# Optimization experiments

Hardware: AMD Instinct MI355X
Metric: run time of the kernel (lower is better)

Reference implementation:

```python
import jax, jax.numpy as jnp
import numpy as np

B, N, M, D, H = 2, 2048, 2048, 1024, 16
HD = D // H          # head_dim = 64
F = int(D * 4.0)     # mlp hidden = 4096
EPS = 1e-5


def layernorm(x, w, b):
    mu = jnp.mean(x, axis=-1, keepdims=True)
    var = jnp.mean(jnp.square(x - mu), axis=-1, keepdims=True)
    return (x - mu) * jax.lax.rsqrt(var + EPS) * w + b


def setup_inputs() -> dict:
    key = jax.random.key(0)
    ks = jax.random.split(key, 8)
    w = lambda k, shape: jax.random.normal(k, shape, dtype=jnp.float32) * 0.02
    return {
        "query": jax.random.normal(ks[0], (B, N, D), dtype=jnp.float32),
        "context": jax.random.normal(ks[1], (B, M, D), dtype=jnp.float32),
        "qpos": jax.random.randint(ks[2], (B, N), 0, N, dtype=jnp.int32),
        "cpos": jax.random.randint(ks[3], (B, M), 0, M, dtype=jnp.int32),
        "Wq_w": w(ks[4], (D, D)), "Wq_b": jnp.zeros((D,), jnp.float32),
        "Wk_w": w(ks[5], (D, D)), "Wk_b": jnp.zeros((D,), jnp.float32),
        "Wv_w": w(ks[6], (D, D)), "Wv_b": jnp.zeros((D,), jnp.float32),
        "qn_w": jnp.ones((HD,), jnp.float32), "qn_b": jnp.zeros((HD,), jnp.float32),
        "kn_w": jnp.ones((HD,), jnp.float32), "kn_b": jnp.zeros((HD,), jnp.float32),
        "ffn_w": jnp.ones((D,), jnp.float32), "ffn_b": jnp.zeros((D,), jnp.float32),
        "fc1_w": w(ks[7], (D, F)), "fc1_b": jnp.zeros((F,), jnp.float32),
        "fc2_w": w(jax.random.fold_in(key, 99), (F, D)), "fc2_b": jnp.zeros((D,), jnp.float32),
    }


def reference(query, context, qpos, cpos,
              Wq_w, Wq_b, Wk_w, Wk_b, Wv_w, Wv_b,
              qn_w, qn_b, kn_w, kn_b,
              ffn_w, ffn_b, fc1_w, fc1_b, fc2_w, fc2_b):
    # rope=None -> qpos/cpos unused (kept for signature fidelity)
    res = query
    # QKV projections, split heads -> (B,H,T,HD)
    Q = (query @ Wq_w + Wq_b).reshape(B, N, H, HD).transpose(0, 2, 1, 3)
    K = (context @ Wk_w + Wk_b).reshape(B, M, H, HD).transpose(0, 2, 1, 3)
    V = (context @ Wv_w + Wv_b).reshape(B, M, H, HD).transpose(0, 2, 1, 3)
    # per-head LayerNorm on q and k
    Q = layernorm(Q, qn_w, qn_b)
    K = layernorm(K, kn_w, kn_b)
    # attention
    scores = jnp.einsum('bhnd,bhmd->bhnm', Q, K) / jnp.sqrt(jnp.float32(HD))
    attn = jax.nn.softmax(scores, axis=-1)
    out = jnp.einsum('bhnm,bhmd->bhnd', attn, V)
    out = out.transpose(0, 2, 1, 3).reshape(B, N, D)
    out = res + out
    # MLP block with pre-norm
    res2 = out
    h = layernorm(out, ffn_w, ffn_b)
    h = jax.nn.gelu(h @ fc1_w + fc1_b, approximate=False)
    h = h @ fc2_w + fc2_b
    return res2 + h
```

## Files before the change

### kernel.cpp

```cpp
#include <hip/hip_runtime.h>
#include <hip/hip_bf16.h>
#include <math.h>

constexpr int Bb  = 2;
constexpr int Nn  = 2048;
constexpr int Mm  = 2048;
constexpr int Dd  = 1024;
constexpr int Hh  = 16;
constexpr int HD  = 64;
constexpr int Ff  = 4096;
constexpr float EPS = 1e-5f;
constexpr float QSCALE = 0.125f * 1.4426950408889634f;
constexpr float SMAX = 12.0f;

typedef __attribute__((ext_vector_type(8))) short bf16x8;
typedef __attribute__((ext_vector_type(4))) short bf16x4;
typedef __attribute__((ext_vector_type(4))) float f32x4;

__device__ inline unsigned short f2bf(float f) {
    __hip_bfloat16 h = __float2bfloat16(f);
    return *reinterpret_cast<unsigned short*>(&h);
}
__device__ inline unsigned short f2bf_rh(float f) {
    union { float f; unsigned u; } c{f};
    return (unsigned short)((c.u + 0x8000u) >> 16);
}
__device__ inline float bf2f(unsigned short u) {
    union { unsigned u; float f; } c{(unsigned)u << 16};
    return c.f;
}

__device__ inline float gelu_fast(float x) {
    float t = x * x;
    float f = fmaf(-0.10295004f, t, -2.30211782f);
    float e = __builtin_amdgcn_exp2f(x * f);
    return x * __builtin_amdgcn_rcpf(1.0f + e);
}

__device__ inline void async_load16(const void* g, void* l) {
    __builtin_amdgcn_global_load_lds(
        (const __attribute__((address_space(1))) void*)g,
        (__attribute__((address_space(3))) void*)l, 16, 0, 0);
}

__device__ inline bf16x8 ld_b64x2(const unsigned short* p) {
    bf16x4 lo = *(const bf16x4*)p;
    bf16x4 hi = *(const bf16x4*)(p + 4);
    bf16x8 r;
#pragma unroll
    for (int i = 0; i < 4; i++) { r[i] = lo[i]; r[i + 4] = hi[i]; }
    return r;
}

__global__ __launch_bounds__(256) void prep_kernel(
    const float* __restrict__ query, const float* __restrict__ context,
    unsigned short* __restrict__ qa, unsigned short* __restrict__ ca,
    const float* __restrict__ W0, const float* __restrict__ W1,
    const float* __restrict__ W2, const float* __restrict__ W3,
    const float* __restrict__ W4,
    unsigned short* __restrict__ T0, unsigned short* __restrict__ T1,
    unsigned short* __restrict__ T2, unsigned short* __restrict__ T3,
    unsigned short* __restrict__ T4)
{
    __shared__ float tile[32][33];
    int bid = blockIdx.x;
    if (bid < 8192) {
        int i = bid * 256 + threadIdx.x;
        const float* x; unsigned short* y; int k;
        if (i < 1048576) { x = query; y = qa; k = i; }
        else { x = context; y = ca; k = i - 1048576; }
        float4 v = reinterpret_cast<const float4*>(x)[k];
        ushort4 o;
        o.x = f2bf(v.x); o.y = f2bf(v.y); o.z = f2bf(v.z); o.w = f2bf(v.w);
        reinterpret_cast<ushort4*>(y)[k] = o;
        return;
    }
    bid -= 8192;
    const float* W; unsigned short* T; int K, Cn, tid;
    if (bid < 3072) {
        int j = bid >> 10; tid = bid & 1023;
        W = (j == 0) ? W0 : (j == 1) ? W1 : W2;
        T = (j == 0) ? T0 : (j == 1) ? T1 : T2;
        K = Dd; Cn = Dd;
    } else if (bid < 7168) {
        tid = bid - 3072; W = W3; T = T3; K = Dd; Cn = Ff;
    } else {
        tid = bid - 7168; W = W4; T = T4; K = Ff; Cn = Dd;
    }
    int xt = Cn >> 5;
    int bx = tid % xt, by = tid / xt;
    int tx = threadIdx.x & 31, ty = threadIdx.x >> 5;
    int c = bx * 32 + tx;
    int kbase = by * 32;
#pragma unroll
    for (int i = ty; i < 32; i += 8)
        tile[i][tx] = W[(size_t)(kbase + i) * Cn + c];
    __syncthreads();
    int k = kbase + tx;
#pragma unroll
    for (int i = ty; i < 32; i += 8)
        T[(size_t)(bx * 32 + i) * K + k] = f2bf(tile[tx][i]);
}

__global__ __launch_bounds__(256) void qkv_fused_kernel(
    const unsigned short* __restrict__ qa, const unsigned short* __restrict__ ca,
    const unsigned short* __restrict__ Wqt, const unsigned short* __restrict__ Wkt,
    const unsigned short* __restrict__ Wvt,
    const float* __restrict__ bq, const float* __restrict__ bk,
    const float* __restrict__ bv,
    const float* __restrict__ qn_w, const float* __restrict__ qn_b,
    const float* __restrict__ kn_w, const float* __restrict__ kn_b,
    unsigned short* __restrict__ Qbh, unsigned short* __restrict__ Kbh,
    unsigned short* __restrict__ Vt_g)
{
    __shared__ __align__(16) unsigned short As[2][128 * 32];
    __shared__ __align__(16) unsigned short Bs[2][128 * 32];

    const int bz = blockIdx.z;
    const unsigned short* A  = (bz == 0) ? qa : ca;
    const unsigned short* Bt = (bz == 0) ? Wqt : (bz == 1) ? Wkt : Wvt;
    const float* bias        = (bz == 0) ? bq  : (bz == 1) ? bk  : bv;
    const int K = Dd;

    const int t    = threadIdx.x;
    const int wave = t >> 6;
    const int lane = t & 63;
    const int r0 = blockIdx.y * 128;
    const int c0 = blockIdx.x * 128;
    const int wm = (wave >> 1) * 64;
    const int wn = (wave & 1) * 64;

    f32x4 acc[4][4];
#pragma unroll
    for (int i = 0; i < 4; i++)
#pragma unroll
        for (int j = 0; j < 4; j++) acc[i][j] = (f32x4)0.0f;

    const int row1 = t >> 2;
    const int kcs  = ((t & 3) ^ ((t >> 3) & 3)) * 8;
    const size_t arow1 = (size_t)(r0 + row1) * K + kcs;
    const size_t arow2 = (size_t)(r0 + row1 + 64) * K + kcs;
    const size_t brow1 = (size_t)(c0 + row1) * K + kcs;
    const size_t brow2 = (size_t)(c0 + row1 + 64) * K + kcs;
    char* A1_0 = (char*)&As[0][0] + wave * 1024;
    char* A2_0 = (char*)&As[0][0] + 4096 + wave * 1024;
    char* B1_0 = (char*)&Bs[0][0] + wave * 1024;
    char* B2_0 = (char*)&Bs[0][0] + 4096 + wave * 1024;
    char* A1_1 = (char*)&As[1][0] + wave * 1024;
    char* A2_1 = (char*)&As[1][0] + 4096 + wave * 1024;
    char* B1_1 = (char*)&Bs[1][0] + wave * 1024;
    char* B2_1 = (char*)&Bs[1][0] + 4096 + wave * 1024;

    const int m   = lane & 15;
    const int swc = ((lane >> 4) ^ ((m >> 1) & 3)) << 3;

    async_load16(A + arow1, A1_0);
    async_load16(A + arow2, A2_0);
    async_load16(Bt + brow1, B1_0);
    async_load16(Bt + brow2, B2_0);

    for (int k0 = 0; k0 < K; k0 += 32) {
        __syncthreads();
        const int cur = (k0 >> 5) & 1;
        if (k0 + 32 < K) {
            const int nk = k0 + 32;
            async_load16(A + arow1 + nk, cur ? A1_0 : A1_1);
            async_load16(A + arow2 + nk, cur ? A2_0 : A2_1);
            async_load16(Bt + brow1 + nk, cur ? B1_0 : B1_1);
            async_load16(Bt + brow2 + nk, cur ? B2_0 : B2_1);
        }
        const unsigned short* Ac = &As[cur][0];
        const unsigned short* Bc = &Bs[cur][0];

        bf16x8 af[4], bfr[4];
#pragma unroll
        for (int mi = 0; mi < 4; mi++)
            af[mi] = *(const bf16x8*)&Ac[(wm + mi * 16 + m) * 32 + swc];
#pragma unroll
        for (int nj = 0; nj < 4; nj++)
            bfr[nj] = *(const bf16x8*)&Bc[(wn + nj * 16 + m) * 32 + swc];
#pragma unroll
        for (int mi = 0; mi < 4; mi++)
#pragma unroll
            for (int nj = 0; nj < 4; nj++)
                acc[mi][nj] = __builtin_amdgcn_mfma_f32_16x16x32_bf16(
                    af[mi], bfr[nj], acc[mi][nj], 0, 0, 0);
    }

    const int rowb = r0 + wm + (lane >> 4) * 4;
    const int colb = c0 + wn + m;
#pragma unroll
    for (int nj = 0; nj < 4; nj++) {
        float bvv = bias[colb + nj * 16];
#pragma unroll
        for (int mi = 0; mi < 4; mi++)
#pragma unroll
            for (int r = 0; r < 4; r++) acc[mi][nj][r] += bvv;
    }

    if (bz < 2) {
        unsigned short* O = (bz == 0) ? Qbh : Kbh;
        const float* lw = (bz == 0) ? qn_w : kn_w;
        const float* lb = (bz == 0) ? qn_b : kn_b;
        const float scale = (bz == 0) ? QSCALE : 1.0f;
        const int hcol = c0 + wn;
        float w4[4], b4[4];
#pragma unroll
        for (int nj = 0; nj < 4; nj++) {
            int d = nj * 16 + m;
            w4[nj] = lw[d]; b4[nj] = lb[d];
        }
#pragma unroll
        for (int mi = 0; mi < 4; mi++) {
#pragma unroll
            for (int r = 0; r < 4; r++) {
                float s = (acc[mi][0][r] + acc[mi][1][r]) +
                          (acc[mi][2][r] + acc[mi][3][r]);
                s += __shfl_xor(s, 1); s += __shfl_xor(s, 2);
                s += __shfl_xor(s, 4); s += __shfl_xor(s, 8);
                float mu = s * (1.0f / 64.0f);
                float v2 = 0.f;
#pragma unroll
                for (int nj = 0; nj < 4; nj++) {
                    float dd = acc[mi][nj][r] - mu; v2 += dd * dd;
                }
                v2 += __shfl_xor(v2, 1); v2 += __shfl_xor(v2, 2);
                v2 += __shfl_xor(v2, 4); v2 += __shfl_xor(v2, 8);
                float rstd = rsqrtf(v2 * (1.0f / 64.0f) + EPS);
                size_t base = (size_t)(rowb + mi * 16 + r) * Dd + hcol;
#pragma unroll
                for (int nj = 0; nj < 4; nj++) {
                    int d = nj * 16 + m;
                    O[base + d] = f2bf(
                        ((acc[mi][nj][r] - mu) * rstd * w4[nj] + b4[nj]) * scale);
                }
            }
        }
    } else {
#pragma unroll
        for (int mi = 0; mi < 4; mi++) {
            int row0 = rowb + mi * 16;
            int bidx = row0 >> 11;
            int mtok = row0 & (Mm - 1);
#pragma unroll
            for (int nj = 0; nj < 4; nj++) {
                int col = colb + nj * 16;
                int h = col >> 6, d = col & 63;
                ushort4 o;
                o.x = f2bf(acc[mi][nj][0]);
                o.y = f2bf(acc[mi][nj][1]);
                o.z = f2bf(acc[mi][nj][2]);
                o.w = f2bf(acc[mi][nj][3]);
                *(ushort4*)(Vt_g + (((size_t)(bidx * Hh + h) * HD + d) << 11) + mtok) = o;
            }
        }
    }
}

template <int EPI, int OUTBF>
__global__ __launch_bounds__(256) void gemm_mfma_bt(
    const unsigned short* __restrict__ A,
    const unsigned short* __restrict__ Bt,
    const float* __restrict__ bias, const float* __restrict__ resid,
    void* __restrict__ Cout, int R, int K, int Cn)
{
    __shared__ __align__(16) unsigned short As[2][128 * 32];
    __shared__ __align__(16) unsigned short Bs[2][128 * 32];

    const int t    = threadIdx.x;
    const int wave = t >> 6;
    const int lane = t & 63;
    const int r0 = blockIdx.y * 128;
    const int c0 = blockIdx.x * 128;
    const int wm = (wave >> 1) * 64;
    const int wn = (wave & 1) * 64;

    f32x4 acc[4][4];
#pragma unroll
    for (int i = 0; i < 4; i++)
#pragma unroll
        for (int j = 0; j < 4; j++) acc[i][j] = (f32x4)0.0f;

    const int row1 = t >> 2;
    const int kcs  = ((t & 3) ^ ((t >> 3) & 3)) * 8;
    const size_t arow1 = (size_t)(r0 + row1) * K + kcs;
    const size_t arow2 = (size_t)(r0 + row1 + 64) * K + kcs;
    const size_t brow1 = (size_t)(c0 + row1) * K + kcs;
    const size_t brow2 = (size_t)(c0 + row1 + 64) * K + kcs;
    char* A1_0 = (char*)&As[0][0] + wave * 1024;
    char* A2_0 = (char*)&As[0][0] + 4096 + wave * 1024;
    char* B1_0 = (char*)&Bs[0][0] + wave * 1024;
    char* B2_0 = (char*)&Bs[0][0] + 4096 + wave * 1024;
    char* A1_1 = (char*)&As[1][0] + wave * 1024;
    char* A2_1 = (char*)&As[1][0] + 4096 + wave * 1024;
    char* B1_1 = (char*)&Bs[1][0] + wave * 1024;
    char* B2_1 = (char*)&Bs[1][0] + 4096 + wave * 1024;

    const int m   = lane & 15;
    const int swc = ((lane >> 4) ^ ((m >> 1) & 3)) << 3;

    async_load16(A + arow1, A1_0);
    async_load16(A + arow2, A2_0);
    async_load16(Bt + brow1, B1_0);
    async_load16(Bt + brow2, B2_0);

    for (int k0 = 0; k0 < K; k0 += 32) {
        __syncthreads();
        const int cur = (k0 >> 5) & 1;
        if (k0 + 32 < K) {
            const int nk = k0 + 32;
            async_load16(A + arow1 + nk, cur ? A1_0 : A1_1);
            async_load16(A + arow2 + nk, cur ? A2_0 : A2_1);
            async_load16(Bt + brow1 + nk, cur ? B1_0 : B1_1);
            async_load16(Bt + brow2 + nk, cur ? B2_0 : B2_1);
        }
        const unsigned short* Ac = &As[cur][0];
        const unsigned short* Bc = &Bs[cur][0];

        bf16x8 af[4], bfr[4];
#pragma unroll
        for (int mi = 0; mi < 4; mi++)
            af[mi] = *(const bf16x8*)&Ac[(wm + mi * 16 + m) * 32 + swc];
#pragma unroll
        for (int nj = 0; nj < 4; nj++)
            bfr[nj] = *(const bf16x8*)&Bc[(wn + nj * 16 + m) * 32 + swc];
#pragma unroll
        for (int mi = 0; mi < 4; mi++)
#pragma unroll
            for (int nj = 0; nj < 4; nj++)
                acc[mi][nj] = __builtin_amdgcn_mfma_f32_16x16x32_bf16(
                    af[mi], bfr[nj], acc[mi][nj], 0, 0, 0);
    }

    const int rowb = r0 + wm + (lane >> 4) * 4;
    const int colb = c0 + wn + m;
#pragma unroll
    for (int mi = 0; mi < 4; mi++) {
#pragma unroll
        for (int nj = 0; nj < 4; nj++) {
            int col = colb + nj * 16;
            float bv = bias[col];
#pragma unroll
            for (int r = 0; r < 4; r++) {
                int row = rowb + mi * 16 + r;
                float v = acc[mi][nj][r] + bv;
                if (EPI == 1) v = gelu_fast(v);
                if (resid) v += resid[(size_t)row * Cn + col];
                if (OUTBF)
                    ((unsigned short*)Cout)[(size_t)row * Cn + col] = f2bf(v);
                else
                    ((float*)Cout)[(size_t)row * Cn + col] = v;
            }
        }
    }
}

__global__ __launch_bounds__(256) void gemm_fc2_split(
    const unsigned short* __restrict__ A,
    const unsigned short* __restrict__ Bt,
    unsigned short* __restrict__ Part)
{
    constexpr int Kfull = Ff;
    constexpr int Ksub  = Ff / 4;
    constexpr int Cn    = Dd;
    const int split = blockIdx.z;
    const int koff  = split * Ksub;

    __shared__ __align__(16) unsigned short As[2][128 * 32];
    __shared__ __align__(16) unsigned short Bs[2][128 * 32];

    const int t    = threadIdx.x;
    const int wave = t >> 6;
    const int lane = t & 63;
    const int r0 = blockIdx.y * 128;
    const int c0 = blockIdx.x * 128;
    const int wm = (wave >> 1) * 64;
    const int wn = (wave & 1) * 64;

    f32x4 acc[4][4];
#pragma unroll
    for (int i = 0; i < 4; i++)
#pragma unroll
        for (int j = 0; j < 4; j++) acc[i][j] = (f32x4)0.0f;

    const int row1 = t >> 2;
    const int kcs  = ((t & 3) ^ ((t >> 3) & 3)) * 8;
    const size_t arow1 = (size_t)(r0 + row1) * Kfull + koff + kcs;
    const size_t arow2 = (size_t)(r0 + row1 + 64) * Kfull + koff + kcs;
    const size_t brow1 = (size_t)(c0 + row1) * Kfull + koff + kcs;
    const size_t brow2 = (size_t)(c0 + row1 + 64) * Kfull + koff + kcs;
    char* A1_0 = (char*)&As[0][0] + wave * 1024;
    char* A2_0 = (char*)&As[0][0] + 4096 + wave * 1024;
    char* B1_0 = (char*)&Bs[0][0] + wave * 1024;
    char* B2_0 = (char*)&Bs[0][0] + 4096 + wave * 1024;
    char* A1_1 = (char*)&As[1][0] + wave * 1024;
    char* A2_1 = (char*)&As[1][0] + 4096 + wave * 1024;
    char* B1_1 = (char*)&Bs[1][0] + wave * 1024;
    char* B2_1 = (char*)&Bs[1][0] + 4096 + wave * 1024;

    const int m   = lane & 15;
    const int swc = ((lane >> 4) ^ ((m >> 1) & 3)) << 3;

    async_load16(A + arow1, A1_0);
    async_load16(A + arow2, A2_0);
    async_load16(Bt + brow1, B1_0);
    async_load16(Bt + brow2, B2_0);

    for (int k0 = 0; k0 < Ksub; k0 += 32) {
        __syncthreads();
        const int cur = (k0 >> 5) & 1;
        if (k0 + 32 < Ksub) {
            const int nk = k0 + 32;
            async_load16(A + arow1 + nk, cur ? A1_0 : A1_1);
            async_load16(A + arow2 + nk, cur ? A2_0 : A2_1);
            async_load16(Bt + brow1 + nk, cur ? B1_0 : B1_1);
            async_load16(Bt + brow2 + nk, cur ? B2_0 : B2_1);
        }
        const unsigned short* Ac = &As[cur][0];
        const unsigned short* Bc = &Bs[cur][0];

        bf16x8 af[4], bfr[4];
#pragma unroll
        for (int mi = 0; mi < 4; mi++)
            af[mi] = *(const bf16x8*)&Ac[(wm + mi * 16 + m) * 32 + swc];
#pragma unroll
        for (int nj = 0; nj < 4; nj++)
            bfr[nj] = *(const bf16x8*)&Bc[(wn + nj * 16 + m) * 32 + swc];
#pragma unroll
        for (int mi = 0; mi < 4; mi++)
#pragma unroll
            for (int nj = 0; nj < 4; nj++)
                acc[mi][nj] = __builtin_amdgcn_mfma_f32_16x16x32_bf16(
                    af[mi], bfr[nj], acc[mi][nj], 0, 0, 0);
    }

    unsigned short* P = Part + (size_t)split * ((size_t)Bb * Nn * Dd);
    const int rowb = r0 + wm + (lane >> 4) * 4;
    const int colb = c0 + wn + m;
#pragma unroll
    for (int mi = 0; mi < 4; mi++)
#pragma unroll
        for (int nj = 0; nj < 4; nj++) {
            int col = colb + nj * 16;
#pragma unroll
            for (int r = 0; r < 4; r++)
                P[(size_t)(rowb + mi * 16 + r) * Cn + col] = f2bf(acc[mi][nj][r]);
        }
}

__global__ __launch_bounds__(256) void fc2_reduce_kernel(
    const unsigned short* __restrict__ Part, const float* __restrict__ bias,
    const float* __restrict__ attn, float* __restrict__ out)
{
    constexpr size_t NEl = (size_t)Bb * Nn * Dd;
    size_t i4 = (size_t)blockIdx.x * 256 + threadIdx.x;
    size_t i = i4 * 4;
    float4 s = *reinterpret_cast<const float4*>(attn + i);
    float4 bv = *reinterpret_cast<const float4*>(bias + (i & (Dd - 1)));
    s.x += bv.x; s.y += bv.y; s.z += bv.z; s.w += bv.w;
#pragma unroll
    for (int sp = 0; sp < 4; sp++) {
        ushort4 u = *reinterpret_cast<const ushort4*>(Part + sp * NEl + i);
        s.x += bf2f(u.x); s.y += bf2f(u.y); s.z += bf2f(u.z); s.w += bf2f(u.w);
    }
    *reinterpret_cast<float4*>(out + i) = s;
}

__global__ __launch_bounds__(256) void ln_row_bf16_kernel(
    const float* __restrict__ X, const float* __restrict__ w,
    const float* __restrict__ b, unsigned short* __restrict__ Y)
{
    int row = blockIdx.x;
    const float* x = X + (size_t)row * Dd;
    int t = threadIdx.x;
    float v[4];
    float s = 0.f;
#pragma unroll
    for (int i = 0; i < 4; i++) { v[i] = x[t + i * 256]; s += v[i]; }
#pragma unroll
    for (int off = 32; off; off >>= 1) s += __shfl_xor(s, off);
    __shared__ float red[4];
    __shared__ float stats[2];
    if ((t & 63) == 0) red[t >> 6] = s;
    __syncthreads();
    if (t == 0) stats[0] = (red[0] + red[1] + red[2] + red[3]) * (1.0f / Dd);
    __syncthreads();
    float mu = stats[0];
    float s2 = 0.f;
#pragma unroll
    for (int i = 0; i < 4; i++) { float d = v[i] - mu; s2 += d * d; }
#pragma unroll
    for (int off = 32; off; off >>= 1) s2 += __shfl_xor(s2, off);
    __syncthreads();
    if ((t & 63) == 0) red[t >> 6] = s2;
    __syncthreads();
    if (t == 0) stats[1] = (red[0] + red[1] + red[2] + red[3]) * (1.0f / Dd);
    __syncthreads();
    float rstd = rsqrtf(stats[1] + EPS);
    unsigned short* y = Y + (size_t)row * Dd;
#pragma unroll
    for (int i = 0; i < 4; i++) {
        int c = t + i * 256;
        y[c] = f2bf((v[i] - mu) * rstd * w[c] + b[c]);
    }
}

__global__ __launch_bounds__(512) void attention_mfma_kernel(
    const unsigned short* __restrict__ Qb,
    const unsigned short* __restrict__ Kb,
    const unsigned short* __restrict__ Vt_g,
    const float* __restrict__ query,
    float* __restrict__ Out)
{
    const int bid = blockIdx.x;
    const int g  = bid & 31;
    const int qt = bid >> 5;
    const int b  = g >> 4;
    const int h  = g & 15;
    const int q0 = qt * 128;

    __shared__ __align__(16) unsigned short Ks[2][2 * 64 * 32];
    __shared__ __align__(16) unsigned short Vts[2][2 * 64 * 32];
    __shared__ __align__(16) unsigned short Ps[8 * 16 * 68];

    const int t    = threadIdx.x;
    const int wave = t >> 6;
    const int lane = t & 63;
    const int m16  = lane & 15;
    const int kg   = lane >> 4;
    const int swc  = (kg ^ ((m16 >> 1) & 3)) << 3;

    bf16x8 qf[2];
    {
        const unsigned short* qp =
            Qb + ((size_t)(b * Nn + q0 + wave * 16 + m16) * Dd + h * HD + kg * 8);
        qf[0] = *(const bf16x8*)qp;
        qf[1] = *(const bf16x8*)(qp + 32);
    }

    f32x4 oacc[4];
    float lrow[4];
#pragma unroll
    for (int i = 0; i < 4; i++) { oacc[i] = (f32x4)0.f; lrow[i] = 0.f; }

    const size_t kbase  = (size_t)(b * Mm) * Dd + h * HD;
    const size_t vtbase = ((size_t)(b * Hh + h) * HD) * Mm;
    unsigned short* psw = Ps + wave * (16 * 68);

    const int u    = t & 255;
    const int pan  = t >> 8;
    const int srow = u >> 2;
    const int schk = ((u & 3) ^ ((srow >> 1) & 3)) * 8;
    char* kdstA = (char*)&Ks[0][0]  + pan * 4096 + (wave & 3) * 1024;
    char* kdstB = (char*)&Ks[1][0]  + pan * 4096 + (wave & 3) * 1024;
    char* vdstA = (char*)&Vts[0][0] + pan * 4096 + (wave & 3) * 1024;
    char* vdstB = (char*)&Vts[1][0] + pan * 4096 + (wave & 3) * 1024;
    const unsigned short* kp0 = Kb + kbase + (size_t)srow * Dd + schk + pan * 32;
    const unsigned short* vp0 = Vt_g + vtbase + (size_t)srow * Mm + schk + pan * 32;

    async_load16(kp0, kdstA);
    async_load16(vp0, vdstA);

    for (int m0 = 0; m0 < Mm; m0 += 64) {
        __syncthreads();
        const int cur = (m0 >> 6) & 1;
        if (m0 + 64 < Mm) {
            async_load16(kp0 + (size_t)(m0 + 64) * Dd, cur ? kdstA : kdstB);
            async_load16(vp0 + (m0 + 64),              cur ? vdstA : vdstB);
        }
        const unsigned short* Kc = &Ks[cur][0];
        const unsigned short* Vc = &Vts[cur][0];

        f32x4 s[4];
#pragma unroll
        for (int j = 0; j < 4; j++) {
            bf16x8 b0 = *(const bf16x8*)&Kc[(j * 16 + m16) * 32 + swc];
            bf16x8 b1 = *(const bf16x8*)&Kc[2048 + (j * 16 + m16) * 32 + swc];
            f32x4 a = (f32x4)(-SMAX);
            a = __builtin_amdgcn_mfma_f32_16x16x32_bf16(qf[0], b0, a, 0, 0, 0);
            a = __builtin_amdgcn_mfma_f32_16x16x32_bf16(qf[1], b1, a, 0, 0, 0);
            s[j] = a;
        }

#pragma unroll
        for (int r = 0; r < 4; r++) {
            float p0 = __builtin_amdgcn_exp2f(s[0][r]);
            float p1 = __builtin_amdgcn_exp2f(s[1][r]);
            float p2 = __builtin_amdgcn_exp2f(s[2][r]);
            float p3 = __builtin_amdgcn_exp2f(s[3][r]);
            lrow[r] += (p0 + p1) + (p2 + p3);
            int qrow = kg * 4 + r;
            psw[qrow * 68 +  0 + m16] = f2bf_rh(p0);
            psw[qrow * 68 + 16 + m16] = f2bf_rh(p1);
            psw[qrow * 68 + 32 + m16] = f2bf_rh(p2);
            psw[qrow * 68 + 48 + m16] = f2bf_rh(p3);
        }

        bf16x8 pf0 = ld_b64x2(psw + m16 * 68 + kg * 8);
        bf16x8 pf1 = ld_b64x2(psw + m16 * 68 + 32 + kg * 8);
#pragma unroll
        for (int dj = 0; dj < 4; dj++) {
            bf16x8 v0 = *(const bf16x8*)&Vc[(dj * 16 + m16) * 32 + swc];
            bf16x8 v1 = *(const bf16x8*)&Vc[2048 + (dj * 16 + m16) * 32 + swc];
            oacc[dj] = __builtin_amdgcn_mfma_f32_16x16x32_bf16(pf0, v0, oacc[dj], 0, 0, 0);
            oacc[dj] = __builtin_amdgcn_mfma_f32_16x16x32_bf16(pf1, v1, oacc[dj], 0, 0, 0);
        }
    }

#pragma unroll
    for (int r = 0; r < 4; r++) {
        float l = lrow[r];
        l += __shfl_xor(l, 1);
        l += __shfl_xor(l, 2);
        l += __shfl_xor(l, 4);
        l += __shfl_xor(l, 8);
        float inv = 1.0f / l;
        const size_t rowbase =
            (size_t)(b * Nn + q0 + wave * 16 + kg * 4 + r) * Dd + h * HD;
#pragma unroll
        for (int dj = 0; dj < 4; dj++) {
            size_t idx = rowbase + dj * 16 + m16;
            Out[idx] = query[idx] + oacc[dj][r] * inv;
        }
    }
}

extern "C" void kernel_launch(void* const* d_in, const int* in_sizes, int n_in,
                              void* d_out, int out_size, void* d_ws, size_t ws_size,
                              hipStream_t stream)
{
    const float* query   = (const float*)d_in[0];
    const float* context = (const float*)d_in[1];
    const float* Wq_w = (const float*)d_in[4];
    const float* Wq_b = (const float*)d_in[5];
    const float* Wk_w = (const float*)d_in[6];
    const float* Wk_b = (const float*)d_in[7];
    const float* Wv_w = (const float*)d_in[8];
    const float* Wv_b = (const float*)d_in[9];
    const float* qn_w = (const float*)d_in[10];
    const float* qn_b = (const float*)d_in[11];
    const float* kn_w = (const float*)d_in[12];
    const float* kn_b = (const float*)d_in[13];
    const float* ffn_w = (const float*)d_in[14];
    const float* ffn_b = (const float*)d_in[15];
    const float* fc1_w = (const float*)d_in[16];
    const float* fc1_b = (const float*)d_in[17];
    const float* fc2_w = (const float*)d_in[18];
    const float* fc2_b = (const float*)d_in[19];

    constexpr size_t BND = (size_t)Bb * Nn * Dd;
    constexpr size_t BMD = (size_t)Bb * Mm * Dd;
    constexpr size_t DD  = (size_t)Dd * Dd;
    constexpr size_t DF  = (size_t)Dd * Ff;

    const size_t need = BND * 4 + (2 * BND + 3 * BMD) * 2 + (3 * DD + 2 * DF) * 2
                      + 4 * BND * 2;
    if (ws_size < need) return;

    char* p = (char*)d_ws;
    float* attn = (float*)p;                   p += BND * 4;
    unsigned short* Qbh  = (unsigned short*)p; p += BND * 2;
    unsigned short* Kbh  = (unsigned short*)p; p += BMD * 2;
    unsigned short* Vt_g = (unsigned short*)p; p += BMD * 2;
    unsigned short* qa   = (unsigned short*)p; p += BND * 2;
    unsigned short* ca   = (unsigned short*)p; p += BMD * 2;
    unsigned short* Wqt  = (unsigned short*)p; p += DD * 2;
    unsigned short* Wkt  = (unsigned short*)p; p += DD * 2;
    unsigned short* Wvt  = (unsigned short*)p; p += DD * 2;
    unsigned short* fc1t = (unsigned short*)p; p += DF * 2;
    unsigned short* fc2t = (unsigned short*)p; p += DF * 2;
    unsigned short* part = (unsigned short*)p; p += 4 * BND * 2;
    unsigned short* normed = Qbh;
    unsigned short* mid    = Kbh;
    float* out = (float*)d_out;

    const int R = Bb * Nn;
    dim3 blk(256);

    prep_kernel<<<19456, blk, 0, stream>>>(
        query, context, qa, ca,
        Wq_w, Wk_w, Wv_w, fc1_w, fc2_w, Wqt, Wkt, Wvt, fc1t, fc2t);

    qkv_fused_kernel<<<dim3(Dd / 128, R / 128, 3), blk, 0, stream>>>(
        qa, ca, Wqt, Wkt, Wvt, Wq_b, Wk_b, Wv_b,
        qn_w, qn_b, kn_w, kn_b, Qbh, Kbh, Vt_g);

    attention_mfma_kernel<<<Bb * Hh * (Nn / 128), 512, 0, stream>>>(
        Qbh, Kbh, Vt_g, query, attn);

    ln_row_bf16_kernel<<<Bb * Nn, blk, 0, stream>>>(attn, ffn_w, ffn_b, normed);

    gemm_mfma_bt<1, 1><<<dim3(Ff / 128, R / 128), blk, 0, stream>>>(
        normed, fc1t, fc1_b, nullptr, mid, R, Dd, Ff);
    gemm_fc2_split<<<dim3(Dd / 128, R / 128, 4), blk, 0, stream>>>(
        mid, fc2t, part);
    fc2_reduce_kernel<<<BND / 4 / 256, blk, 0, stream>>>(
        part, fc2_b, attn, out);
}
```

Measured before the change: 367.3 us.

## Triple-buffer GEMM and attention LDS pipelines and remap blocks for XCD locality

Converts the double-buffered async-load loops in the QKV, FC1, FC2 and attention kernels into three-stage pipelines. Each iteration now waits with an explicit vmcnt and a raw barrier, replacing a full __syncthreads, so two tiles stay in flight. All GEMM launches become 1D grids with a block-index remap, taking lid&7 as a chunk id, so that blocks which likely land on the same XCD share A/B row panels in L2. This uses 50% more LDS per block, which may reduce occupancy, and relies on hand-written waitcnt counts being correct.

```diff
diff --git a/kernel.cpp b/kernel.cpp
--- a/kernel.cpp
+++ b/kernel.cpp
@@ -113,10 +113,17 @@
     unsigned short* __restrict__ Qbh, unsigned short* __restrict__ Kbh,
     unsigned short* __restrict__ Vt_g)
 {
-    __shared__ __align__(16) unsigned short As[2][128 * 32];
-    __shared__ __align__(16) unsigned short Bs[2][128 * 32];
-
-    const int bz = blockIdx.z;
+    __shared__ __align__(16) unsigned short As[3][128 * 32];
+    __shared__ __align__(16) unsigned short Bs[3][128 * 32];
+
+    const int lid    = blockIdx.x;
+    const int chunk  = lid & 7;
+    const int within = lid >> 3;
+    const int bx     = within & 7;
+    const int rest   = within >> 3;
+    const int bz     = rest >> 2;
+    const int by     = chunk * 4 + (rest & 3);
+
     const unsigned short* A  = (bz == 0) ? qa : ca;
     const unsigned short* Bt = (bz == 0) ? Wqt : (bz == 1) ? Wkt : Wvt;
     const float* bias        = (bz == 0) ? bq  : (bz == 1) ? bk  : bv;
@@ -125,8 +132,8 @@
     const int t    = threadIdx.x;
     const int wave = t >> 6;
     const int lane = t & 63;
-    const int r0 = blockIdx.y * 128;
-    const int c0 = blockIdx.x * 128;
+    const int r0 = by * 128;
+    const int c0 = bx * 128;
     const int wm = (wave >> 1) * 64;
     const int wn = (wave & 1) * 64;
 
@@ -142,36 +149,22 @@
     const size_t arow2 = (size_t)(r0 + row1 + 64) * K + kcs;
     const size_t brow1 = (size_t)(c0 + row1) * K + kcs;
     const size_t brow2 = (size_t)(c0 + row1 + 64) * K + kcs;
-    char* A1_0 = (char*)&As[0][0] + wave * 1024;
-    char* A2_0 = (char*)&As[0][0] + 4096 + wave * 1024;
-    char* B1_0 = (char*)&Bs[0][0] + wave * 1024;
-    char* B2_0 = (char*)&Bs[0][0] + 4096 + wave * 1024;
-    char* A1_1 = (char*)&As[1][0] + wave * 1024;
-    char* A2_1 = (char*)&As[1][0] + 4096 + wave * 1024;
-    char* B1_1 = (char*)&Bs[1][0] + wave * 1024;
-    char* B2_1 = (char*)&Bs[1][0] + 4096 + wave * 1024;
 
     const int m   = lane & 15;
     const int swc = ((lane >> 4) ^ ((m >> 1) & 3)) << 3;
 
-    async_load16(A + arow1, A1_0);
-    async_load16(A + arow2, A2_0);
-    async_load16(Bt + brow1, B1_0);
-    async_load16(Bt + brow2, B2_0);
-
-    for (int k0 = 0; k0 < K; k0 += 32) {
-        __syncthreads();
-        const int cur = (k0 >> 5) & 1;
-        if (k0 + 32 < K) {
-            const int nk = k0 + 32;
-            async_load16(A + arow1 + nk, cur ? A1_0 : A1_1);
-            async_load16(A + arow2 + nk, cur ? A2_0 : A2_1);
-            async_load16(Bt + brow1 + nk, cur ? B1_0 : B1_1);
-            async_load16(Bt + brow2 + nk, cur ? B2_0 : B2_1);
-        }
-        const unsigned short* Ac = &As[cur][0];
-        const unsigned short* Bc = &Bs[cur][0];
-
+    auto stage = [&](int kt, int b) {
+        const int nk = kt * 32;
+        char* ab = (char*)&As[b][0] + wave * 1024;
+        char* bb = (char*)&Bs[b][0] + wave * 1024;
+        async_load16(A + arow1 + nk, ab);
+        async_load16(A + arow2 + nk, ab + 4096);
+        async_load16(Bt + brow1 + nk, bb);
+        async_load16(Bt + brow2 + nk, bb + 4096);
+    };
+    auto compute = [&](int b) {
+        const unsigned short* Ac = &As[b][0];
+        const unsigned short* Bc = &Bs[b][0];
         bf16x8 af[4], bfr[4];
 #pragma unroll
         for (int mi = 0; mi < 4; mi++)
@@ -185,7 +178,23 @@
             for (int nj = 0; nj < 4; nj++)
                 acc[mi][nj] = __builtin_amdgcn_mfma_f32_16x16x32_bf16(
                     af[mi], bfr[nj], acc[mi][nj], 0, 0, 0);
-    }
+    };
+
+    const int NT = K >> 5;
+    stage(0, 0);
+    stage(1, 1);
+    int bc = 0, bn = 2;
+    for (int kt = 0; kt < NT - 1; ++kt) {
+        asm volatile("s_waitcnt vmcnt(4)" ::: "memory");
+        __builtin_amdgcn_s_barrier();
+        if (kt + 2 < NT) stage(kt + 2, bn);
+        compute(bc);
+        bc = (bc == 2) ? 0 : bc + 1;
+        bn = (bn == 2) ? 0 : bn + 1;
+    }
+    asm volatile("s_waitcnt vmcnt(0)" ::: "memory");
+    __builtin_amdgcn_s_barrier();
+    compute(bc);
 
     const int rowb = r0 + wm + (lane >> 4) * 4;
     const int colb = c0 + wn + m;
@@ -264,14 +273,20 @@
     const float* __restrict__ bias, const float* __restrict__ resid,
     void* __restrict__ Cout, int R, int K, int Cn)
 {
-    __shared__ __align__(16) unsigned short As[2][128 * 32];
-    __shared__ __align__(16) unsigned short Bs[2][128 * 32];
+    __shared__ __align__(16) unsigned short As[3][128 * 32];
+    __shared__ __align__(16) unsigned short Bs[3][128 * 32];
+
+    const int lid    = blockIdx.x;
+    const int chunk  = lid & 7;
+    const int within = lid >> 3;
+    const int bx     = (chunk & 3) * 8 + (within & 7);
+    const int by     = (chunk >> 2) * 16 + (within >> 3);
 
     const int t    = threadIdx.x;
     const int wave = t >> 6;
     const int lane = t & 63;
-    const int r0 = blockIdx.y * 128;
-    const int c0 = blockIdx.x * 128;
+    const int r0 = by * 128;
+    const int c0 = bx * 128;
     const int wm = (wave >> 1) * 64;
     const int wn = (wave & 1) * 64;
 
@@ -287,36 +302,22 @@
     const size_t arow2 = (size_t)(r0 + row1 + 64) * K + kcs;
     const size_t brow1 = (size_t)(c0 + row1) * K + kcs;
     const size_t brow2 = (size_t)(c0 + row1 + 64) * K + kcs;
-    char* A1_0 = (char*)&As[0][0] + wave * 1024;
-    char* A2_0 = (char*)&As[0][0] + 4096 + wave * 1024;
-    char* B1_0 = (char*)&Bs[0][0] + wave * 1024;
-    char* B2_0 = (char*)&Bs[0][0] + 4096 + wave * 1024;
-    char* A1_1 = (char*)&As[1][0] + wave * 1024;
-    char* A2_1 = (char*)&As[1][0] + 4096 + wave * 1024;
-    char* B1_1 = (char*)&Bs[1][0] + wave * 1024;
-    char* B2_1 = (char*)&Bs[1][0] + 4096 + wave * 1024;
 
     const int m   = lane & 15;
     const int swc = ((lane >> 4) ^ ((m >> 1) & 3)) << 3;
 
-    async_load16(A + arow1, A1_0);
-    async_load16(A + arow2, A2_0);
-    async_load16(Bt + brow1, B1_0);
-    async_load16(Bt + brow2, B2_0);
-
-    for (int k0 = 0; k0 < K; k0 += 32) {
-        __syncthreads();
-        const int cur = (k0 >> 5) & 1;
-        if (k0 + 32 < K) {
-            const int nk = k0 + 32;
-            async_load16(A + arow1 + nk, cur ? A1_0 : A1_1);
-            async_load16(A + arow2 + nk, cur ? A2_0 : A2_1);
-            async_load16(Bt + brow1 + nk, cur ? B1_0 : B1_1);
-            async_load16(Bt + brow2 + nk, cur ? B2_0 : B2_1);
-        }
-        const unsigned short* Ac = &As[cur][0];
-        const unsigned short* Bc = &Bs[cur][0];
-
+    auto stage = [&](int kt, int b) {
+        const int nk = kt * 32;
+        char* ab = (char*)&As[b][0] + wave * 1024;
+        char* bb = (char*)&Bs[b][0] + wave * 1024;
+        async_load16(A + arow1 + nk, ab);
+        async_load16(A + arow2 + nk, ab + 4096);
+        async_load16(Bt + brow1 + nk, bb);
+        async_load16(Bt + brow2 + nk, bb + 4096);
+    };
+    auto compute = [&](int b) {
+        const unsigned short* Ac = &As[b][0];
+        const unsigned short* Bc = &Bs[b][0];
         bf16x8 af[4], bfr[4];
 #pragma unroll
         for (int mi = 0; mi < 4; mi++)
@@ -330,7 +331,23 @@
             for (int nj = 0; nj < 4; nj++)
                 acc[mi][nj] = __builtin_amdgcn_mfma_f32_16x16x32_bf16(
                     af[mi], bfr[nj], acc[mi][nj], 0, 0, 0);
-    }
+    };
+
+    const int NT = K >> 5;
+    stage(0, 0);
+    if (NT > 1) stage(1, 1);
+    int bc = 0, bn = 2;
+    for (int kt = 0; kt < NT - 1; ++kt) {
+        asm volatile("s_waitcnt vmcnt(4)" ::: "memory");
+        __builtin_amdgcn_s_barrier();
+        if (kt + 2 < NT) stage(kt + 2, bn);
+        compute(bc);
+        bc = (bc == 2) ? 0 : bc + 1;
+        bn = (bn == 2) ? 0 : bn + 1;
+    }
+    asm volatile("s_waitcnt vmcnt(0)" ::: "memory");
+    __builtin_amdgcn_s_barrier();
+    compute(bc);
 
     const int rowb = r0 + wm + (lane >> 4) * 4;
     const int colb = c0 + wn + m;
@@ -363,17 +380,24 @@
     constexpr int Kfull = Ff;
     constexpr int Ksub  = Ff / 4;
     constexpr int Cn    = Dd;
-    const int split = blockIdx.z;
-    const int koff  = split * Ksub;
-
-    __shared__ __align__(16) unsigned short As[2][128 * 32];
-    __shared__ __align__(16) unsigned short Bs[2][128 * 32];
+
+    __shared__ __align__(16) unsigned short As[3][128 * 32];
+    __shared__ __align__(16) unsigned short Bs[3][128 * 32];
+
+    const int lid    = blockIdx.x;
+    const int chunk  = lid & 7;
+    const int within = lid >> 3;
+    const int bx     = within & 7;
+    const int rest   = within >> 3;
+    const int split  = chunk >> 1;
+    const int by     = (chunk & 1) * 16 + rest;
+    const int koff   = split * Ksub;
 
     const int t    = threadIdx.x;
     const int wave = t >> 6;
     const int lane = t & 63;
-    const int r0 = blockIdx.y * 128;
-    const int c0 = blockIdx.x * 128;
+    const int r0 = by * 128;
+    const int c0 = bx * 128;
     const int wm = (wave >> 1) * 64;
     const int wn = (wave & 1) * 64;
 
@@ -389,36 +413,22 @@
     const size_t arow2 = (size_t)(r0 + row1 + 64) * Kfull + koff + kcs;
     const size_t brow1 = (size_t)(c0 + row1) * Kfull + koff + kcs;
     const size_t brow2 = (size_t)(c0 + row1 + 64) * Kfull + koff + kcs;
-    char* A1_0 = (char*)&As[0][0] + wave * 1024;
-    char* A2_0 = (char*)&As[0][0] + 4096 + wave * 1024;
-    char* B1_0 = (char*)&Bs[0][0] + wave * 1024;
-    char* B2_0 = (char*)&Bs[0][0] + 4096 + wave * 1024;
-    char* A1_1 = (char*)&As[1][0] + wave * 1024;
-    char* A2_1 = (char*)&As[1][0] + 4096 + wave * 1024;
-    char* B1_1 = (char*)&Bs[1][0] + wave * 1024;
-    char* B2_1 = (char*)&Bs[1][0] + 4096 + wave * 1024;
 
     const int m   = lane & 15;
     const int swc = ((lane >> 4) ^ ((m >> 1) & 3)) << 3;
 
-    async_load16(A + arow1, A1_0);
-    async_load16(A + arow2, A2_0);
-    async_load16(Bt + brow1, B1_0);
-    async_load16(Bt + brow2, B2_0);
-
-    for (int k0 = 0; k0 < Ksub; k0 += 32) {
-        __syncthreads();
-        const int cur = (k0 >> 5) & 1;
-        if (k0 + 32 < Ksub) {
-            const int nk = k0 + 32;
-            async_load16(A + arow1 + nk, cur ? A1_0 : A1_1);
-            async_load16(A + arow2 + nk, cur ? A2_0 : A2_1);
-            async_load16(Bt + brow1 + nk, cur ? B1_0 : B1_1);
-            async_load16(Bt + brow2 + nk, cur ? B2_0 : B2_1);
-        }
-        const unsigned short* Ac = &As[cur][0];
-        const unsigned short* Bc = &Bs[cur][0];
-
+    auto stage = [&](int kt, int b) {
+        const int nk = kt * 32;
+        char* ab = (char*)&As[b][0] + wave * 1024;
+        char* bb = (char*)&Bs[b][0] + wave * 1024;
+        async_load16(A + arow1 + nk, ab);
+        async_load16(A + arow2 + nk, ab + 4096);
+        async_load16(Bt + brow1 + nk, bb);
+        async_load16(Bt + brow2 + nk, bb + 4096);
+    };
+    auto compute = [&](int b) {
+        const unsigned short* Ac = &As[b][0];
+        const unsigned short* Bc = &Bs[b][0];
         bf16x8 af[4], bfr[4];
 #pragma unroll
         for (int mi = 0; mi < 4; mi++)
@@ -432,7 +442,23 @@
             for (int nj = 0; nj < 4; nj++)
                 acc[mi][nj] = __builtin_amdgcn_mfma_f32_16x16x32_bf16(
                     af[mi], bfr[nj], acc[mi][nj], 0, 0, 0);
-    }
+    };
+
+    const int NT = Ksub >> 5;
+    stage(0, 0);
+    stage(1, 1);
+    int bc = 0, bn = 2;
+    for (int kt = 0; kt < NT - 1; ++kt) {
+        asm volatile("s_waitcnt vmcnt(4)" ::: "memory");
+        __builtin_amdgcn_s_barrier();
+        if (kt + 2 < NT) stage(kt + 2, bn);
+        compute(bc);
+        bc = (bc == 2) ? 0 : bc + 1;
+        bn = (bn == 2) ? 0 : bn + 1;
+    }
+    asm volatile("s_waitcnt vmcnt(0)" ::: "memory");
+    __builtin_amdgcn_s_barrier();
+    compute(bc);
 
     unsigned short* P = Part + (size_t)split * ((size_t)Bb * Nn * Dd);
     const int rowb = r0 + wm + (lane >> 4) * 4;
@@ -519,8 +545,8 @@
     const int h  = g & 15;
     const int q0 = qt * 128;
 
-    __shared__ __align__(16) unsigned short Ks[2][2 * 64 * 32];
-    __shared__ __align__(16) unsigned short Vts[2][2 * 64 * 32];
+    __shared__ __align__(16) unsigned short Ks[3][2 * 64 * 32];
+    __shared__ __align__(16) unsigned short Vts[3][2 * 64 * 32];
     __shared__ __align__(16) unsigned short Ps[8 * 16 * 68];
 
     const int t    = threadIdx.x;
@@ -551,25 +577,18 @@
     const int pan  = t >> 8;
     const int srow = u >> 2;
     const int schk = ((u & 3) ^ ((srow >> 1) & 3)) * 8;
-    char* kdstA = (char*)&Ks[0][0]  + pan * 4096 + (wave & 3) * 1024;
-    char* kdstB = (char*)&Ks[1][0]  + pan * 4096 + (wave & 3) * 1024;
-    char* vdstA = (char*)&Vts[0][0] + pan * 4096 + (wave & 3) * 1024;
-    char* vdstB = (char*)&Vts[1][0] + pan * 4096 + (wave & 3) * 1024;
     const unsigned short* kp0 = Kb + kbase + (size_t)srow * Dd + schk + pan * 32;
     const unsigned short* vp0 = Vt_g + vtbase + (size_t)srow * Mm + schk + pan * 32;
 
-    async_load16(kp0, kdstA);
-    async_load16(vp0, vdstA);
-
-    for (int m0 = 0; m0 < Mm; m0 += 64) {
-        __syncthreads();
-        const int cur = (m0 >> 6) & 1;
-        if (m0 + 64 < Mm) {
-            async_load16(kp0 + (size_t)(m0 + 64) * Dd, cur ? kdstA : kdstB);
-            async_load16(vp0 + (m0 + 64),              cur ? vdstA : vdstB);
-        }
-        const unsigned short* Kc = &Ks[cur][0];
-        const unsigned short* Vc = &Vts[cur][0];
+    auto stageKV = [&](int mt, int bf) {
+        char* kd = (char*)&Ks[bf][0]  + pan * 4096 + (wave & 3) * 1024;
+        char* vd = (char*)&Vts[bf][0] + pan * 4096 + (wave & 3) * 1024;
+        async_load16(kp0 + (size_t)(mt * 64) * Dd, kd);
+        async_load16(vp0 + mt * 64, vd);
+    };
+    auto computeTile = [&](int bf) {
+        const unsigned short* Kc = &Ks[bf][0];
+        const unsigned short* Vc = &Vts[bf][0];
 
         f32x4 s[4];
 #pragma unroll
@@ -605,7 +624,23 @@
             oacc[dj] = __builtin_amdgcn_mfma_f32_16x16x32_bf16(pf0, v0, oacc[dj], 0, 0, 0);
             oacc[dj] = __builtin_amdgcn_mfma_f32_16x16x32_bf16(pf1, v1, oacc[dj], 0, 0, 0);
         }
-    }
+    };
+
+    const int NT = Mm / 64;
+    stageKV(0, 0);
+    stageKV(1, 1);
+    int bc = 0, bn = 2;
+    for (int tt = 0; tt < NT - 1; ++tt) {
+        asm volatile("s_waitcnt vmcnt(2)" ::: "memory");
+        __builtin_amdgcn_s_barrier();
+        if (tt + 2 < NT) stageKV(tt + 2, bn);
+        computeTile(bc);
+        bc = (bc == 2) ? 0 : bc + 1;
+        bn = (bn == 2) ? 0 : bn + 1;
+    }
+    asm volatile("s_waitcnt vmcnt(0)" ::: "memory");
+    __builtin_amdgcn_s_barrier();
+    computeTile(bc);
 
 #pragma unroll
     for (int r = 0; r < 4; r++) {
@@ -681,7 +716,7 @@
         query, context, qa, ca,
         Wq_w, Wk_w, Wv_w, fc1_w, fc2_w, Wqt, Wkt, Wvt, fc1t, fc2t);
 
-    qkv_fused_kernel<<<dim3(Dd / 128, R / 128, 3), blk, 0, stream>>>(
+    qkv_fused_kernel<<<768, blk, 0, stream>>>(
         qa, ca, Wqt, Wkt, Wvt, Wq_b, Wk_b, Wv_b,
         qn_w, qn_b, kn_w, kn_b, Qbh, Kbh, Vt_g);
 
@@ -690,9 +725,9 @@
 
     ln_row_bf16_kernel<<<Bb * Nn, blk, 0, stream>>>(attn, ffn_w, ffn_b, normed);
 
-    gemm_mfma_bt<1, 1><<<dim3(Ff / 128, R / 128), blk, 0, stream>>>(
+    gemm_mfma_bt<1, 1><<<1024, blk, 0, stream>>>(
         normed, fc1t, fc1_b, nullptr, mid, R, Dd, Ff);
-    gemm_fc2_split<<<dim3(Dd / 128, R / 128, 4), blk, 0, stream>>>(
+    gemm_fc2_split<<<1024, blk, 0, stream>>>(
         mid, fc2t, part);
     fc2_reduce_kernel<<<BND / 4 / 256, blk, 0, stream>>>(
         part, fc2_b, attn, out);
```

Result: slower. 381.6 us (+3.9%).
